# Kernel optimization log

Hardware: AMD Instinct MI355X
Metric: run time of the kernel (lower is better)

The kernel has to match this reference:

```python
import jax, jax.numpy as jnp
import numpy as np

B, N, C = 8, 4096, 512
K = 512   # key_channels
V = 512   # value_channels (must equal in_channels for reprojection to typecheck)
H = 8     # head_count


def setup_inputs() -> dict:
    key = jax.random.key(0)
    ks = jax.random.split(key, 10)
    s = 1.0 / np.sqrt(C)
    return {
        "input_": jax.random.normal(ks[0], (B, N, C), jnp.float32),
        "y": jax.random.normal(ks[1], (B, N, C), jnp.float32),
        "Wk": jax.random.uniform(ks[2], (C, K), jnp.float32, -s, s),
        "bk": jax.random.uniform(ks[3], (K,), jnp.float32, -s, s),
        "Wq": jax.random.uniform(ks[4], (C, K), jnp.float32, -s, s),
        "bq": jax.random.uniform(ks[5], (K,), jnp.float32, -s, s),
        "Wv": jax.random.uniform(ks[6], (C, K), jnp.float32, -s, s),
        "bv": jax.random.uniform(ks[7], (K,), jnp.float32, -s, s),
        "Wr": jax.random.uniform(ks[8], (C, K), jnp.float32, -s, s),
        "br": jax.random.uniform(ks[9], (K,), jnp.float32, -s, s),
    }


def reference(input_, y, Wk, bk, Wq, bq, Wv, bv, Wr, br):
    hk = K // H  # head key channels
    hv = V // H  # head value channels
    # projections -> [B, N, H, h]
    keys = ((input_ + y) @ Wk + bk).reshape(B, N, H, hk)
    queries = (y @ Wq + bq).reshape(B, N, H, hk)
    values = (input_ @ Wv + bv).reshape(B, N, H, hv)
    # key softmax over tokens N; query softmax over head channels hk
    keys = jax.nn.softmax(keys, axis=1)
    queries = jax.nn.softmax(queries, axis=3)
    # context[b,h,k,v] = sum_n key[b,n,h,k] * value[b,n,h,v]
    context = jnp.einsum('bnhk,bnhv->bhkv', keys, values)
    # attended[b,n,h,v] = sum_k context[b,h,k,v] * query[b,n,h,k]
    attended = jnp.einsum('bhkv,bnhk->bnhv', context, queries)
    aggregated = attended.reshape(B, N, V)  # concat heads over value channels
    return aggregated @ Wr + br
```

## Files before the change

### kernel.cpp

```cpp
#include <hip/hip_runtime.h>
#include <hip/hip_bf16.h>
#include <stdint.h>


typedef __attribute__((ext_vector_type(8))) short short8;
typedef __attribute__((ext_vector_type(4))) float f32x4;
typedef __attribute__((ext_vector_type(4))) unsigned short us4;

__device__ __forceinline__ unsigned short f2bf(float f) {
  union { float f; unsigned u; } v; v.f = f;
  unsigned r = v.u + 0x7FFFu + ((v.u >> 16) & 1u);
  return (unsigned short)(r >> 16);
}
__device__ __forceinline__ float bf2f(unsigned short u) {
  union { unsigned u; float f; } v; v.u = ((unsigned)u) << 16;
  return v.f;
}
__device__ __forceinline__ ushort2 pk2(float a, float b) {
  __hip_bfloat162 h = __float22bfloat162_rn(float2{a, b});
  return *reinterpret_cast<ushort2*>(&h);
}
__device__ __forceinline__ void gload16(const void* g, void* l) {
  __builtin_amdgcn_global_load_lds(
      (const __attribute__((address_space(1))) void*)g,
      (__attribute__((address_space(3))) void*)l, 16, 0, 0);
}

__global__ void prep_w(const float* __restrict__ Wk, const float* __restrict__ Wq,
                       const float* __restrict__ Wv, const float* __restrict__ Wr,
                       unsigned short* __restrict__ Wt) {
  __shared__ float tile[64][65];
  const int t = threadIdx.x;
  const int bx = blockIdx.x, by = blockIdx.y, w = blockIdx.z;
  const float* W = (w == 0) ? Wk : (w == 1) ? Wq : (w == 2) ? Wv : Wr;
  unsigned short* O = Wt + (size_t)w * 512 * 512;
#pragma unroll
  for (int p = 0; p < 16; ++p) {
    int idx = p * 256 + t; int r = idx >> 6, c = idx & 63;
    tile[r][c] = W[(size_t)(by * 64 + r) * 512 + bx * 64 + c];
  }
  __syncthreads();
#pragma unroll
  for (int p = 0; p < 16; ++p) {
    int idx = p * 256 + t; int r = idx >> 6, c = idx & 63;
    O[(size_t)(bx * 64 + r) * 512 + by * 64 + c] = f2bf(tile[c][r]);
  }
}

__global__ __launch_bounds__(256) void prep_xy(const float* __restrict__ x, const float* __restrict__ y,
                        unsigned short* __restrict__ xb, unsigned short* __restrict__ yb,
                        unsigned short* __restrict__ xyb) {
  const size_t i = ((size_t)blockIdx.x * 256 + threadIdx.x) * 16;
  float4 a[4], b[4];
#pragma unroll
  for (int q = 0; q < 4; ++q) a[q] = *(const float4*)(x + i + q * 4);
#pragma unroll
  for (int q = 0; q < 4; ++q) b[q] = *(const float4*)(y + i + q * 4);
#pragma unroll
  for (int h = 0; h < 2; ++h) {
    float4 a0 = a[2 * h], a1 = a[2 * h + 1], b0 = b[2 * h], b1 = b[2 * h + 1];
    short8 vx, vy, vs;
    ushort2 p;
    p = pk2(a0.x, a0.y); vx[0] = (short)p.x; vx[1] = (short)p.y;
    p = pk2(a0.z, a0.w); vx[2] = (short)p.x; vx[3] = (short)p.y;
    p = pk2(a1.x, a1.y); vx[4] = (short)p.x; vx[5] = (short)p.y;
    p = pk2(a1.z, a1.w); vx[6] = (short)p.x; vx[7] = (short)p.y;
    p = pk2(b0.x, b0.y); vy[0] = (short)p.x; vy[1] = (short)p.y;
    p = pk2(b0.z, b0.w); vy[2] = (short)p.x; vy[3] = (short)p.y;
    p = pk2(b1.x, b1.y); vy[4] = (short)p.x; vy[5] = (short)p.y;
    p = pk2(b1.z, b1.w); vy[6] = (short)p.x; vy[7] = (short)p.y;
    p = pk2(a0.x + b0.x, a0.y + b0.y); vs[0] = (short)p.x; vs[1] = (short)p.y;
    p = pk2(a0.z + b0.z, a0.w + b0.w); vs[2] = (short)p.x; vs[3] = (short)p.y;
    p = pk2(a1.x + b1.x, a1.y + b1.y); vs[4] = (short)p.x; vs[5] = (short)p.y;
    p = pk2(a1.z + b1.z, a1.w + b1.w); vs[6] = (short)p.x; vs[7] = (short)p.y;
    *(short8*)(xb + i + h * 8) = vx;
    *(short8*)(yb + i + h * 8) = vy;
    *(short8*)(xyb + i + h * 8) = vs;
  }
}

__global__ __launch_bounds__(256) void gemm_proj3(
    const unsigned short* __restrict__ xyb, const unsigned short* __restrict__ xb,
    const unsigned short* __restrict__ yb, const unsigned short* __restrict__ Wt,
    const float* __restrict__ bk, const float* __restrict__ bv, const float* __restrict__ bq,
    unsigned short* __restrict__ KeT, unsigned short* __restrict__ VT,
    unsigned short* __restrict__ Qp, float* __restrict__ S, int sec_off) {
  __shared__ __align__(16) unsigned short As[2][128][64];
  __shared__ __align__(16) unsigned short Bs[2][128][64];
  const int t = threadIdx.x, l = t & 63, w = t >> 6;
  const int lr = l & 15, lg = l >> 4;
  const int wr = w >> 1, wc = w & 1;
  const int sec = (int)(blockIdx.x >> 10) + sec_off;
  const int bid = blockIdx.x & 1023;
  const int swz = (bid & 7) * 128 + (bid >> 3);
  const int tn = swz & 3, tm = swz >> 2;

  const unsigned short* A = (sec == 0) ? xyb : (sec == 1) ? xb : yb;
  const unsigned short* Bbase = Wt + (size_t)((sec == 0) ? 0 : (sec == 1) ? 2 : 1) * 262144;
  const float* bias = (sec == 0) ? bk : (sec == 1) ? bv : bq;

  const int r0 = w * 8 + (l >> 3);
  const int su = ((l & 7) ^ (l >> 3)) * 8;
  const unsigned short* Ag = A + (size_t)(tm * 128 + r0) * 512 + su;
  const unsigned short* Bg = Bbase + (size_t)(tn * 128 + r0) * 512 + su;

  f32x4 acc[4][4] = {};

#define PSTAGE(buf, kt)                                                        \
  {                                                                            \
    _Pragma("unroll") for (int i = 0; i < 4; ++i) {                            \
      gload16(Ag + (size_t)i * 32 * 512 + (kt) * 64, &As[buf][i * 32 + w * 8][0]); \
      gload16(Bg + (size_t)i * 32 * 512 + (kt) * 64, &Bs[buf][i * 32 + w * 8][0]); \
    }                                                                          \
  }

  PSTAGE(0, 0)
  PSTAGE(1, 1)
  for (int kt = 0; kt < 8; ++kt) {
    const int cur = kt & 1;
    if (kt < 7) { asm volatile("s_waitcnt vmcnt(8)" ::: "memory"); }
    else        { asm volatile("s_waitcnt vmcnt(0)" ::: "memory"); }
    __builtin_amdgcn_s_barrier();
    asm volatile("" ::: "memory");
    __builtin_amdgcn_s_setprio(1);
#pragma unroll
    for (int kk = 0; kk < 2; ++kk) {
      short8 af[4], bf[4];
#pragma unroll
      for (int m = 0; m < 4; ++m)
        af[m] = *(const short8*)&As[cur][wr * 64 + m * 16 + lr][((kk * 4 + lg) ^ (lr & 7)) * 8];
#pragma unroll
      for (int n = 0; n < 4; ++n)
        bf[n] = *(const short8*)&Bs[cur][wc * 64 + n * 16 + lr][((kk * 4 + lg) ^ (lr & 7)) * 8];
#pragma unroll
      for (int m = 0; m < 4; ++m)
#pragma unroll
        for (int n = 0; n < 4; ++n)
          acc[m][n] = __builtin_amdgcn_mfma_f32_16x16x32_bf16(af[m], bf[n], acc[m][n], 0, 0, 0);
    }
    __builtin_amdgcn_s_setprio(0);
    asm volatile("" ::: "memory");
    __builtin_amdgcn_s_barrier();
    asm volatile("" ::: "memory");
    if (kt < 6) PSTAGE(cur, kt + 2)
  }
#undef PSTAGE

  const int c_base = tn * 128 + wc * 64;
  const int r_base = tm * 128 + wr * 64;
  float bv_[4];
#pragma unroll
  for (int n = 0; n < 4; ++n) bv_[n] = bias[c_base + n * 16 + lr];

  if (sec == 2) {
#pragma unroll
    for (int m = 0; m < 4; ++m) {
#pragma unroll
      for (int j = 0; j < 4; ++j) {
        float a0 = acc[m][0][j] + bv_[0], a1 = acc[m][1][j] + bv_[1];
        float a2 = acc[m][2][j] + bv_[2], a3 = acc[m][3][j] + bv_[3];
        float mx = fmaxf(fmaxf(a0, a1), fmaxf(a2, a3));
#pragma unroll
        for (int o = 1; o < 16; o <<= 1) mx = fmaxf(mx, __shfl_xor(mx, o));
        float e0 = __expf(a0 - mx), e1 = __expf(a1 - mx);
        float e2 = __expf(a2 - mx), e3 = __expf(a3 - mx);
        float s = e0 + e1 + e2 + e3;
#pragma unroll
        for (int o = 1; o < 16; o <<= 1) s += __shfl_xor(s, o);
        const float rs = 1.0f / s;
        const int row = r_base + m * 16 + lg * 4 + j;
        Qp[(size_t)row * 512 + c_base + 0 * 16 + lr] = f2bf(e0 * rs);
        Qp[(size_t)row * 512 + c_base + 1 * 16 + lr] = f2bf(e1 * rs);
        Qp[(size_t)row * 512 + c_base + 2 * 16 + lr] = f2bf(e2 * rs);
        Qp[(size_t)row * 512 + c_base + 3 * 16 + lr] = f2bf(e3 * rs);
      }
    }
  } else if (sec == 0) {
    const int b = (tm * 128) >> 12;
#pragma unroll
    for (int n = 0; n < 4; ++n) {
      const int col = c_base + n * 16 + lr;
      float srow = 0.f;
#pragma unroll
      for (int m = 0; m < 4; ++m) {
        const int row = r_base + m * 16 + lg * 4;
        const int nl = row & 4095;
        us4 v;
#pragma unroll
        for (int j = 0; j < 4; ++j) {
          float f = __expf(acc[m][n][j] + bv_[n]);
          srow += f;
          v[j] = f2bf(f);
        }
        *(us4*)&KeT[((size_t)(b * 512 + col)) * 4096 + nl] = v;
      }
      srow += __shfl_xor(srow, 16);
      srow += __shfl_xor(srow, 32);
      if (lg == 0) atomicAdd(&S[b * 512 + col], srow);
    }
  } else {
    const int b = (tm * 128) >> 12;
#pragma unroll
    for (int n = 0; n < 4; ++n) {
      const int col = c_base + n * 16 + lr;
#pragma unroll
      for (int m = 0; m < 4; ++m) {
        const int row = r_base + m * 16 + lg * 4;
        const int nl = row & 4095;
        us4 v;
#pragma unroll
        for (int j = 0; j < 4; ++j) v[j] = f2bf(acc[m][n][j] + bv_[n]);
        *(us4*)&VT[((size_t)(b * 512 + col)) * 4096 + nl] = v;
      }
    }
  }
}

__global__ void context_partial(const unsigned short* __restrict__ KeT,
                                const unsigned short* __restrict__ VT,
                                float* __restrict__ cp) {
  const int t = threadIdx.x, l = t & 63, w = t >> 6;
  const int lr = l & 15, lg = l >> 4;
  const int ch = blockIdx.x, h = blockIdx.y, b = blockIdx.z;
  const unsigned short* Kp = KeT + ((size_t)b * 512 + h * 64) * 4096;
  const unsigned short* Vp = VT + ((size_t)b * 512 + h * 64) * 4096;
  const int tok_w = ch * 1024 + w * 256;
  f32x4 acc[4][4] = {};
  for (int s = 0; s < 8; ++s) {
    const int tok = tok_w + s * 32 + lg * 8;
    short8 a[4], kf[4];
#pragma unroll
    for (int m = 0; m < 4; ++m) a[m] = *(const short8*)&Vp[(size_t)(m * 16 + lr) * 4096 + tok];
#pragma unroll
    for (int n = 0; n < 4; ++n) kf[n] = *(const short8*)&Kp[(size_t)(n * 16 + lr) * 4096 + tok];
#pragma unroll
    for (int m = 0; m < 4; ++m)
#pragma unroll
      for (int n = 0; n < 4; ++n)
        acc[m][n] = __builtin_amdgcn_mfma_f32_16x16x32_bf16(a[m], kf[n], acc[m][n], 0, 0, 0);
  }
  __shared__ float red[4][64][64];
#pragma unroll
  for (int m = 0; m < 4; ++m)
#pragma unroll
    for (int n = 0; n < 4; ++n)
#pragma unroll
      for (int j = 0; j < 4; ++j)
        red[w][m * 16 + lg * 4 + j][n * 16 + lr] = acc[m][n][j];
  __syncthreads();
  const int blk = (b * 8 + h) * 4 + ch;
  float* o = cp + (size_t)blk * 4096;
  for (int i = 0; i < 16; ++i) {
    int e = i * 256 + t;
    int v = e >> 6, k = e & 63;
    o[e] = red[0][v][k] + red[1][v][k] + red[2][v][k] + red[3][v][k];
  }
}

__global__ void ctx_reduce(const float* __restrict__ cp, const float* __restrict__ S,
                           unsigned short* __restrict__ ctxN) {
  const int bh = blockIdx.x, t = threadIdx.x;
  const float* p = cp + (size_t)bh * 4 * 4096;
  for (int i = 0; i < 16; ++i) {
    int e = i * 256 + t;
    float vsum = p[e] + p[4096 + e] + p[8192 + e] + p[12288 + e];
    int v = e >> 6, k = e & 63;
    ctxN[(size_t)bh * 4096 + k * 64 + v] = f2bf(vsum / S[bh * 64 + k]);
  }
}

__global__ void ctx_mm(const unsigned short* __restrict__ ctxN, const unsigned short* __restrict__ Wrt,
                       unsigned short* __restrict__ MT) {
  const int t = threadIdx.x, l = t & 63, w = t >> 6;
  const int lr = l & 15, lg = l >> 4;
  const int h = blockIdx.x, b = blockIdx.y;
  const unsigned short* Ap = ctxN + (size_t)(b * 8 + h) * 4096;
  f32x4 acc[4][8] = {};
  const int c0 = w * 128;
#pragma unroll
  for (int kk = 0; kk < 2; ++kk) {
    const int vb = kk * 32 + lg * 8;
    short8 a[4], bfr[8];
#pragma unroll
    for (int m = 0; m < 4; ++m) a[m] = *(const short8*)&Ap[(m * 16 + lr) * 64 + vb];
#pragma unroll
    for (int n = 0; n < 8; ++n) bfr[n] = *(const short8*)&Wrt[(size_t)(c0 + n * 16 + lr) * 512 + h * 64 + vb];
#pragma unroll
    for (int m = 0; m < 4; ++m)
#pragma unroll
      for (int n = 0; n < 8; ++n)
        acc[m][n] = __builtin_amdgcn_mfma_f32_16x16x32_bf16(a[m], bfr[n], acc[m][n], 0, 0, 0);
  }
#pragma unroll
  for (int n = 0; n < 8; ++n) {
    const int c = c0 + n * 16 + lr;
#pragma unroll
    for (int m = 0; m < 4; ++m) {
      const int k = m * 16 + lg * 4;
      us4 v;
#pragma unroll
      for (int j = 0; j < 4; ++j) v[j] = f2bf(acc[m][n][j]);
      *(us4*)&MT[((size_t)b * 512 + c) * 512 + h * 64 + k] = v;
    }
  }
}

__global__ __launch_bounds__(256) void gemm_final(const unsigned short* __restrict__ Qs,
                           const unsigned short* __restrict__ MT,
                           const float* __restrict__ br, float* __restrict__ out) {
  __shared__ __align__(16) unsigned short As[2][128][64];
  __shared__ __align__(16) unsigned short Bs[2][128][64];
  const int t = threadIdx.x, l = t & 63, w = t >> 6;
  const int lr = l & 15, lg = l >> 4;
  const int wr = w >> 1, wc = w & 1;
  const int bid = blockIdx.x;
  const int swz = (bid & 7) * 128 + (bid >> 3);
  const int tn = swz & 3, tm = swz >> 2;

  const unsigned short* Bbase = MT + (size_t)(tm >> 5) * 262144;
  const int r0 = w * 8 + (l >> 3);
  const int su = ((l & 7) ^ (l >> 3)) * 8;
  const unsigned short* Ag = Qs + (size_t)(tm * 128 + r0) * 512 + su;
  const unsigned short* Bg = Bbase + (size_t)(tn * 128 + r0) * 512 + su;

  f32x4 acc[4][4] = {};

#define PSTAGE(buf, kt)                                                        \
  {                                                                            \
    _Pragma("unroll") for (int i = 0; i < 4; ++i) {                            \
      gload16(Ag + (size_t)i * 32 * 512 + (kt) * 64, &As[buf][i * 32 + w * 8][0]); \
      gload16(Bg + (size_t)i * 32 * 512 + (kt) * 64, &Bs[buf][i * 32 + w * 8][0]); \
    }                                                                          \
  }

  PSTAGE(0, 0)
  PSTAGE(1, 1)
  for (int kt = 0; kt < 8; ++kt) {
    const int cur = kt & 1;
    if (kt < 7) { asm volatile("s_waitcnt vmcnt(8)" ::: "memory"); }
    else        { asm volatile("s_waitcnt vmcnt(0)" ::: "memory"); }
    __builtin_amdgcn_s_barrier();
    asm volatile("" ::: "memory");
    __builtin_amdgcn_s_setprio(1);
#pragma unroll
    for (int kk = 0; kk < 2; ++kk) {
      short8 af[4], bf[4];
#pragma unroll
      for (int m = 0; m < 4; ++m)
        af[m] = *(const short8*)&As[cur][wr * 64 + m * 16 + lr][((kk * 4 + lg) ^ (lr & 7)) * 8];
#pragma unroll
      for (int n = 0; n < 4; ++n)
        bf[n] = *(const short8*)&Bs[cur][wc * 64 + n * 16 + lr][((kk * 4 + lg) ^ (lr & 7)) * 8];
#pragma unroll
      for (int m = 0; m < 4; ++m)
#pragma unroll
        for (int n = 0; n < 4; ++n)
          acc[m][n] = __builtin_amdgcn_mfma_f32_16x16x32_bf16(af[m], bf[n], acc[m][n], 0, 0, 0);
    }
    __builtin_amdgcn_s_setprio(0);
    asm volatile("" ::: "memory");
    __builtin_amdgcn_s_barrier();
    asm volatile("" ::: "memory");
    if (kt < 6) PSTAGE(cur, kt + 2)
  }
#undef PSTAGE

  const int c_base = tn * 128 + wc * 64;
  const int r_base = tm * 128 + wr * 64;
#pragma unroll
  for (int n = 0; n < 4; ++n) {
    const int col = c_base + n * 16 + lr;
    const float bs = br[col];
#pragma unroll
    for (int m = 0; m < 4; ++m) {
      const int row = r_base + m * 16 + lg * 4;
#pragma unroll
      for (int j = 0; j < 4; ++j)
        out[(size_t)(row + j) * 512 + col] = acc[m][n][j] + bs;
    }
  }
}

extern "C" void kernel_launch(void* const* d_in, const int* in_sizes, int n_in,
                              void* d_out, int out_size, void* d_ws, size_t ws_size,
                              hipStream_t stream) {
  (void)in_sizes; (void)n_in; (void)out_size;
  const float* x  = (const float*)d_in[0];
  const float* y  = (const float*)d_in[1];
  const float* Wk = (const float*)d_in[2];
  const float* bk = (const float*)d_in[3];
  const float* Wq = (const float*)d_in[4];
  const float* bq = (const float*)d_in[5];
  const float* Wv = (const float*)d_in[6];
  const float* bv = (const float*)d_in[7];
  const float* Wr = (const float*)d_in[8];
  const float* br = (const float*)d_in[9];
  float* out = (float*)d_out;

  char* ws = (char*)d_ws;
  unsigned short* Wt   = (unsigned short*)(ws + 0);
  unsigned short* xb   = (unsigned short*)(ws + 2097152);
  unsigned short* yb   = (unsigned short*)(ws + 35651584);
  unsigned short* xyb  = (unsigned short*)(ws + 69206016);
  unsigned short* KeT  = (unsigned short*)(ws + 102760448);
  unsigned short* VT   = (unsigned short*)(ws + 136314880);
  float* S             = (float*)(ws + 169869312);
  float* cp            = (float*)(ws + 169885696);
  unsigned short* ctxN = (unsigned short*)(ws + 174080000);
  unsigned short* MT   = (unsigned short*)(ws + 174604288);
  unsigned short* QpX  = (unsigned short*)(ws + 178798592);
  const bool wide = ws_size >= (size_t)210364416;
  unsigned short* Qp   = wide ? QpX : xyb;

  prep_w<<<dim3(8, 8, 4), 256, 0, stream>>>(Wk, Wq, Wv, Wr, Wt);
  prep_xy<<<4096, 256, 0, stream>>>(x, y, xb, yb, xyb);
  hipMemsetAsync(S, 0, 512 * 8 * sizeof(float), stream);
  if (wide) {
    gemm_proj3<<<3072, 256, 0, stream>>>(xyb, xb, yb, Wt, bk, bv, bq, KeT, VT, Qp, S, 0);
  } else {
    gemm_proj3<<<2048, 256, 0, stream>>>(xyb, xb, yb, Wt, bk, bv, bq, KeT, VT, Qp, S, 0);
    gemm_proj3<<<1024, 256, 0, stream>>>(xyb, xb, yb, Wt, bk, bv, bq, KeT, VT, Qp, S, 2);
  }
  context_partial<<<dim3(4, 8, 8), 256, 0, stream>>>(KeT, VT, cp);
  ctx_reduce<<<64, 256, 0, stream>>>(cp, S, ctxN);
  ctx_mm<<<dim3(8, 8), 256, 0, stream>>>(ctxN, Wt + 3 * 262144, MT);
  gemm_final<<<1024, 256, 0, stream>>>(Qp, MT, br, out);
}
```

Baseline: 223.5 us.

## Fuse fp32-to-bf16 input conversion and x+y add into projection GEMM loads

```diff
diff --git a/kernel.cpp b/kernel.cpp
--- a/kernel.cpp
+++ b/kernel.cpp
@@ -47,61 +47,210 @@
   }
 }
 
-__global__ __launch_bounds__(256) void prep_xy(const float* __restrict__ x, const float* __restrict__ y,
-                        unsigned short* __restrict__ xb, unsigned short* __restrict__ yb,
-                        unsigned short* __restrict__ xyb) {
-  const size_t i = ((size_t)blockIdx.x * 256 + threadIdx.x) * 16;
-  float4 a[4], b[4];
-#pragma unroll
-  for (int q = 0; q < 4; ++q) a[q] = *(const float4*)(x + i + q * 4);
-#pragma unroll
-  for (int q = 0; q < 4; ++q) b[q] = *(const float4*)(y + i + q * 4);
-#pragma unroll
-  for (int h = 0; h < 2; ++h) {
-    float4 a0 = a[2 * h], a1 = a[2 * h + 1], b0 = b[2 * h], b1 = b[2 * h + 1];
-    short8 vx, vy, vs;
-    ushort2 p;
-    p = pk2(a0.x, a0.y); vx[0] = (short)p.x; vx[1] = (short)p.y;
-    p = pk2(a0.z, a0.w); vx[2] = (short)p.x; vx[3] = (short)p.y;
-    p = pk2(a1.x, a1.y); vx[4] = (short)p.x; vx[5] = (short)p.y;
-    p = pk2(a1.z, a1.w); vx[6] = (short)p.x; vx[7] = (short)p.y;
-    p = pk2(b0.x, b0.y); vy[0] = (short)p.x; vy[1] = (short)p.y;
-    p = pk2(b0.z, b0.w); vy[2] = (short)p.x; vy[3] = (short)p.y;
-    p = pk2(b1.x, b1.y); vy[4] = (short)p.x; vy[5] = (short)p.y;
-    p = pk2(b1.z, b1.w); vy[6] = (short)p.x; vy[7] = (short)p.y;
-    p = pk2(a0.x + b0.x, a0.y + b0.y); vs[0] = (short)p.x; vs[1] = (short)p.y;
-    p = pk2(a0.z + b0.z, a0.w + b0.w); vs[2] = (short)p.x; vs[3] = (short)p.y;
-    p = pk2(a1.x + b1.x, a1.y + b1.y); vs[4] = (short)p.x; vs[5] = (short)p.y;
-    p = pk2(a1.z + b1.z, a1.w + b1.w); vs[6] = (short)p.x; vs[7] = (short)p.y;
-    *(short8*)(xb + i + h * 8) = vx;
-    *(short8*)(yb + i + h * 8) = vy;
-    *(short8*)(xyb + i + h * 8) = vs;
-  }
-}
-
-__global__ __launch_bounds__(256) void gemm_proj3(
-    const unsigned short* __restrict__ xyb, const unsigned short* __restrict__ xb,
-    const unsigned short* __restrict__ yb, const unsigned short* __restrict__ Wt,
-    const float* __restrict__ bk, const float* __restrict__ bv, const float* __restrict__ bq,
-    unsigned short* __restrict__ KeT, unsigned short* __restrict__ VT,
-    unsigned short* __restrict__ Qp, float* __restrict__ S, int sec_off) {
+template <int MODE>
+__global__ __launch_bounds__(256) void gemm_projf(
+    const float* __restrict__ A0, const float* __restrict__ A1,
+    const unsigned short* __restrict__ Bt, const float* __restrict__ bias,
+    unsigned short* __restrict__ Out, float* __restrict__ S) {
   __shared__ __align__(16) unsigned short As[2][128][64];
   __shared__ __align__(16) unsigned short Bs[2][128][64];
   const int t = threadIdx.x, l = t & 63, w = t >> 6;
   const int lr = l & 15, lg = l >> 4;
   const int wr = w >> 1, wc = w & 1;
-  const int sec = (int)(blockIdx.x >> 10) + sec_off;
-  const int bid = blockIdx.x & 1023;
+  const int bid = blockIdx.x;
   const int swz = (bid & 7) * 128 + (bid >> 3);
   const int tn = swz & 3, tm = swz >> 2;
 
-  const unsigned short* A = (sec == 0) ? xyb : (sec == 1) ? xb : yb;
-  const unsigned short* Bbase = Wt + (size_t)((sec == 0) ? 0 : (sec == 1) ? 2 : 1) * 262144;
-  const float* bias = (sec == 0) ? bk : (sec == 1) ? bv : bq;
-
   const int r0 = w * 8 + (l >> 3);
   const int su = ((l & 7) ^ (l >> 3)) * 8;
-  const unsigned short* Ag = A + (size_t)(tm * 128 + r0) * 512 + su;
+  const unsigned short* Bg = Bt + (size_t)(tn * 128 + r0) * 512 + su;
+
+  const int ar = t >> 1, ah = t & 1;
+  const float* Ar0 = A0 + (size_t)(tm * 128 + ar) * 512 + ah * 32;
+  const float* Ar1 = (MODE == 0) ? (A1 + (size_t)(tm * 128 + ar) * 512 + ah * 32) : nullptr;
+
+  float4 ax[8], ay[8];
+  f32x4 acc[4][4] = {};
+
+#define FENCE asm volatile("" ::: "memory")
+#define ALOAD(kt)                                                              \
+  {                                                                            \
+    _Pragma("unroll") for (int i = 0; i < 8; ++i)                              \
+        ax[i] = *(const float4*)(Ar0 + (kt) * 64 + i * 4);                     \
+    if (MODE == 0) {                                                           \
+      _Pragma("unroll") for (int i = 0; i < 8; ++i)                            \
+          ay[i] = *(const float4*)(Ar1 + (kt) * 64 + i * 4);                   \
+    }                                                                          \
+  }
+#define AWRITE(buf)                                                            \
+  {                                                                            \
+    _Pragma("unroll") for (int iu = 0; iu < 4; ++iu) {                         \
+      float4 u0 = ax[2 * iu], u1 = ax[2 * iu + 1];                             \
+      if (MODE == 0) {                                                         \
+        float4 v0 = ay[2 * iu], v1 = ay[2 * iu + 1];                           \
+        u0.x += v0.x; u0.y += v0.y; u0.z += v0.z; u0.w += v0.w;                \
+        u1.x += v1.x; u1.y += v1.y; u1.z += v1.z; u1.w += v1.w;                \
+      }                                                                        \
+      ushort2 c0 = pk2(u0.x, u0.y), c1 = pk2(u0.z, u0.w);                      \
+      ushort2 c2 = pk2(u1.x, u1.y), c3 = pk2(u1.z, u1.w);                      \
+      short8 v;                                                                \
+      v[0] = (short)c0.x; v[1] = (short)c0.y; v[2] = (short)c1.x;              \
+      v[3] = (short)c1.y; v[4] = (short)c2.x; v[5] = (short)c2.y;              \
+      v[6] = (short)c3.x; v[7] = (short)c3.y;                                  \
+      *(short8*)&As[buf][ar][(((ah * 4 + iu) ^ (ar & 7)) * 8)] = v;            \
+    }                                                                          \
+  }
+#define BGISS(buf, kt)                                                         \
+  {                                                                            \
+    _Pragma("unroll") for (int i = 0; i < 4; ++i)                              \
+        gload16(Bg + (size_t)i * 32 * 512 + (kt) * 64, &Bs[buf][i * 32 + w * 8][0]); \
+  }
+#define WAIT_A asm volatile("s_waitcnt vmcnt(4)" ::: "memory")
+#define WAIT_B                                                                 \
+  {                                                                            \
+    if (MODE == 0) { asm volatile("s_waitcnt vmcnt(24)" ::: "memory"); }       \
+    else           { asm volatile("s_waitcnt vmcnt(16)" ::: "memory"); }       \
+  }
+
+  ALOAD(0); FENCE; BGISS(0, 0);
+  WAIT_A;
+  AWRITE(0);
+  FENCE; ALOAD(1); FENCE; BGISS(1, 1);
+  asm volatile("s_waitcnt lgkmcnt(0)" ::: "memory");
+  WAIT_B;
+  __builtin_amdgcn_s_barrier();
+  FENCE;
+
+  for (int kt = 0; kt < 8; ++kt) {
+    const int cur = kt & 1;
+    __builtin_amdgcn_s_setprio(1);
+#pragma unroll
+    for (int kk = 0; kk < 2; ++kk) {
+      short8 af[4], bf[4];
+#pragma unroll
+      for (int m = 0; m < 4; ++m)
+        af[m] = *(const short8*)&As[cur][wr * 64 + m * 16 + lr][((kk * 4 + lg) ^ (lr & 7)) * 8];
+#pragma unroll
+      for (int n = 0; n < 4; ++n)
+        bf[n] = *(const short8*)&Bs[cur][wc * 64 + n * 16 + lr][((kk * 4 + lg) ^ (lr & 7)) * 8];
+#pragma unroll
+      for (int m = 0; m < 4; ++m)
+#pragma unroll
+        for (int n = 0; n < 4; ++n)
+          acc[m][n] = __builtin_amdgcn_mfma_f32_16x16x32_bf16(af[m], bf[n], acc[m][n], 0, 0, 0);
+    }
+    __builtin_amdgcn_s_setprio(0);
+    FENCE;
+    if (kt < 7) {
+      WAIT_A;
+      AWRITE(cur ^ 1);
+      asm volatile("s_waitcnt lgkmcnt(0)" ::: "memory");
+      __builtin_amdgcn_s_barrier();
+      FENCE;
+      if (kt < 6) {
+        ALOAD(kt + 2); FENCE; BGISS(cur, kt + 2);
+        WAIT_B;
+      } else {
+        asm volatile("s_waitcnt vmcnt(0)" ::: "memory");
+      }
+      __builtin_amdgcn_s_barrier();
+      FENCE;
+    }
+  }
+  asm volatile("s_waitcnt vmcnt(0) lgkmcnt(0)" ::: "memory");
+#undef FENCE
+#undef ALOAD
+#undef AWRITE
+#undef BGISS
+#undef WAIT_A
+#undef WAIT_B
+
+  const int c_base = tn * 128 + wc * 64;
+  const int r_base = tm * 128 + wr * 64;
+  float bv_[4];
+#pragma unroll
+  for (int n = 0; n < 4; ++n) bv_[n] = bias[c_base + n * 16 + lr];
+
+  if (MODE == 1) {
+#pragma unroll
+    for (int m = 0; m < 4; ++m) {
+#pragma unroll
+      for (int j = 0; j < 4; ++j) {
+        float a0 = acc[m][0][j] + bv_[0], a1 = acc[m][1][j] + bv_[1];
+        float a2 = acc[m][2][j] + bv_[2], a3 = acc[m][3][j] + bv_[3];
+        float mx = fmaxf(fmaxf(a0, a1), fmaxf(a2, a3));
+#pragma unroll
+        for (int o = 1; o < 16; o <<= 1) mx = fmaxf(mx, __shfl_xor(mx, o));
+        float e0 = __expf(a0 - mx), e1 = __expf(a1 - mx);
+        float e2 = __expf(a2 - mx), e3 = __expf(a3 - mx);
+        float s = e0 + e1 + e2 + e3;
+#pragma unroll
+        for (int o = 1; o < 16; o <<= 1) s += __shfl_xor(s, o);
+        const float rs = 1.0f / s;
+        const int row = r_base + m * 16 + lg * 4 + j;
+        Out[(size_t)row * 512 + c_base + 0 * 16 + lr] = f2bf(e0 * rs);
+        Out[(size_t)row * 512 + c_base + 1 * 16 + lr] = f2bf(e1 * rs);
+        Out[(size_t)row * 512 + c_base + 2 * 16 + lr] = f2bf(e2 * rs);
+        Out[(size_t)row * 512 + c_base + 3 * 16 + lr] = f2bf(e3 * rs);
+      }
+    }
+  } else if (MODE == 0) {
+    const int b = (tm * 128) >> 12;
+#pragma unroll
+    for (int n = 0; n < 4; ++n) {
+      const int col = c_base + n * 16 + lr;
+      float srow = 0.f;
+#pragma unroll
+      for (int m = 0; m < 4; ++m) {
+        const int row = r_base + m * 16 + lg * 4;
+        const int nl = row & 4095;
+        us4 v;
+#pragma unroll
+        for (int j = 0; j < 4; ++j) {
+          float f = __expf(acc[m][n][j] + bv_[n]);
+          srow += f;
+          v[j] = f2bf(f);
+        }
+        *(us4*)&Out[((size_t)(b * 512 + col)) * 4096 + nl] = v;
+      }
+      srow += __shfl_xor(srow, 16);
+      srow += __shfl_xor(srow, 32);
+      if (lg == 0) atomicAdd(&S[b * 512 + col], srow);
+    }
+  } else {
+    const int b = (tm * 128) >> 12;
+#pragma unroll
+    for (int n = 0; n < 4; ++n) {
+      const int col = c_base + n * 16 + lr;
+#pragma unroll
+      for (int m = 0; m < 4; ++m) {
+        const int row = r_base + m * 16 + lg * 4;
+        const int nl = row & 4095;
+        us4 v;
+#pragma unroll
+        for (int j = 0; j < 4; ++j) v[j] = f2bf(acc[m][n][j] + bv_[n]);
+        *(us4*)&Out[((size_t)(b * 512 + col)) * 4096 + nl] = v;
+      }
+    }
+  }
+}
+
+__global__ __launch_bounds__(256) void gemm_final(const unsigned short* __restrict__ Qs,
+                           const unsigned short* __restrict__ MT,
+                           const float* __restrict__ br, float* __restrict__ out) {
+  __shared__ __align__(16) unsigned short As[2][128][64];
+  __shared__ __align__(16) unsigned short Bs[2][128][64];
+  const int t = threadIdx.x, l = t & 63, w = t >> 6;
+  const int lr = l & 15, lg = l >> 4;
+  const int wr = w >> 1, wc = w & 1;
+  const int bid = blockIdx.x;
+  const int swz = (bid & 7) * 128 + (bid >> 3);
+  const int tn = swz & 3, tm = swz >> 2;
+
+  const unsigned short* Bbase = MT + (size_t)(tm >> 5) * 262144;
+  const int r0 = w * 8 + (l >> 3);
+  const int su = ((l & 7) ^ (l >> 3)) * 8;
+  const unsigned short* Ag = Qs + (size_t)(tm * 128 + r0) * 512 + su;
   const unsigned short* Bg = Bbase + (size_t)(tn * 128 + r0) * 512 + su;
 
   f32x4 acc[4][4] = {};
@@ -148,70 +297,16 @@
 
   const int c_base = tn * 128 + wc * 64;
   const int r_base = tm * 128 + wr * 64;
-  float bv_[4];
-#pragma unroll
-  for (int n = 0; n < 4; ++n) bv_[n] = bias[c_base + n * 16 + lr];
-
-  if (sec == 2) {
+#pragma unroll
+  for (int n = 0; n < 4; ++n) {
+    const int col = c_base + n * 16 + lr;
+    const float bs = br[col];
 #pragma unroll
     for (int m = 0; m < 4; ++m) {
-#pragma unroll
-      for (int j = 0; j < 4; ++j) {
-        float a0 = acc[m][0][j] + bv_[0], a1 = acc[m][1][j] + bv_[1];
-        float a2 = acc[m][2][j] + bv_[2], a3 = acc[m][3][j] + bv_[3];
-        float mx = fmaxf(fmaxf(a0, a1), fmaxf(a2, a3));
-#pragma unroll
-        for (int o = 1; o < 16; o <<= 1) mx = fmaxf(mx, __shfl_xor(mx, o));
-        float e0 = __expf(a0 - mx), e1 = __expf(a1 - mx);
-        float e2 = __expf(a2 - mx), e3 = __expf(a3 - mx);
-        float s = e0 + e1 + e2 + e3;
-#pragma unroll
-        for (int o = 1; o < 16; o <<= 1) s += __shfl_xor(s, o);
-        const float rs = 1.0f / s;
-        const int row = r_base + m * 16 + lg * 4 + j;
-        Qp[(size_t)row * 512 + c_base + 0 * 16 + lr] = f2bf(e0 * rs);
-        Qp[(size_t)row * 512 + c_base + 1 * 16 + lr] = f2bf(e1 * rs);
-        Qp[(size_t)row * 512 + c_base + 2 * 16 + lr] = f2bf(e2 * rs);
-        Qp[(size_t)row * 512 + c_base + 3 * 16 + lr] = f2bf(e3 * rs);
-      }
-    }
-  } else if (sec == 0) {
-    const int b = (tm * 128) >> 12;
-#pragma unroll
-    for (int n = 0; n < 4; ++n) {
-      const int col = c_base + n * 16 + lr;
-      float srow = 0.f;
-#pragma unroll
-      for (int m = 0; m < 4; ++m) {
-        const int row = r_base + m * 16 + lg * 4;
-        const int nl = row & 4095;
-        us4 v;
-#pragma unroll
-        for (int j = 0; j < 4; ++j) {
-          float f = __expf(acc[m][n][j] + bv_[n]);
-          srow += f;
-          v[j] = f2bf(f);
-        }
-        *(us4*)&KeT[((size_t)(b * 512 + col)) * 4096 + nl] = v;
-      }
-      srow += __shfl_xor(srow, 16);
-      srow += __shfl_xor(srow, 32);
-      if (lg == 0) atomicAdd(&S[b * 512 + col], srow);
-    }
-  } else {
-    const int b = (tm * 128) >> 12;
-#pragma unroll
-    for (int n = 0; n < 4; ++n) {
-      const int col = c_base + n * 16 + lr;
-#pragma unroll
-      for (int m = 0; m < 4; ++m) {
-        const int row = r_base + m * 16 + lg * 4;
-        const int nl = row & 4095;
-        us4 v;
-#pragma unroll
-        for (int j = 0; j < 4; ++j) v[j] = f2bf(acc[m][n][j] + bv_[n]);
-        *(us4*)&VT[((size_t)(b * 512 + col)) * 4096 + nl] = v;
-      }
+      const int row = r_base + m * 16 + lg * 4;
+#pragma unroll
+      for (int j = 0; j < 4; ++j)
+        out[(size_t)(row + j) * 512 + col] = acc[m][n][j] + bs;
     }
   }
 }
@@ -305,86 +400,10 @@
   }
 }
 
-__global__ __launch_bounds__(256) void gemm_final(const unsigned short* __restrict__ Qs,
-                           const unsigned short* __restrict__ MT,
-                           const float* __restrict__ br, float* __restrict__ out) {
-  __shared__ __align__(16) unsigned short As[2][128][64];
-  __shared__ __align__(16) unsigned short Bs[2][128][64];
-  const int t = threadIdx.x, l = t & 63, w = t >> 6;
-  const int lr = l & 15, lg = l >> 4;
-  const int wr = w >> 1, wc = w & 1;
-  const int bid = blockIdx.x;
-  const int swz = (bid & 7) * 128 + (bid >> 3);
-  const int tn = swz & 3, tm = swz >> 2;
-
-  const unsigned short* Bbase = MT + (size_t)(tm >> 5) * 262144;
-  const int r0 = w * 8 + (l >> 3);
-  const int su = ((l & 7) ^ (l >> 3)) * 8;
-  const unsigned short* Ag = Qs + (size_t)(tm * 128 + r0) * 512 + su;
-  const unsigned short* Bg = Bbase + (size_t)(tn * 128 + r0) * 512 + su;
-
-  f32x4 acc[4][4] = {};
-
-#define PSTAGE(buf, kt)                                                        \
-  {                                                                            \
-    _Pragma("unroll") for (int i = 0; i < 4; ++i) {                            \
-      gload16(Ag + (size_t)i * 32 * 512 + (kt) * 64, &As[buf][i * 32 + w * 8][0]); \
-      gload16(Bg + (size_t)i * 32 * 512 + (kt) * 64, &Bs[buf][i * 32 + w * 8][0]); \
-    }                                                                          \
-  }
-
-  PSTAGE(0, 0)
-  PSTAGE(1, 1)
-  for (int kt = 0; kt < 8; ++kt) {
-    const int cur = kt & 1;
-    if (kt < 7) { asm volatile("s_waitcnt vmcnt(8)" ::: "memory"); }
-    else        { asm volatile("s_waitcnt vmcnt(0)" ::: "memory"); }
-    __builtin_amdgcn_s_barrier();
-    asm volatile("" ::: "memory");
-    __builtin_amdgcn_s_setprio(1);
-#pragma unroll
-    for (int kk = 0; kk < 2; ++kk) {
-      short8 af[4], bf[4];
-#pragma unroll
-      for (int m = 0; m < 4; ++m)
-        af[m] = *(const short8*)&As[cur][wr * 64 + m * 16 + lr][((kk * 4 + lg) ^ (lr & 7)) * 8];
-#pragma unroll
-      for (int n = 0; n < 4; ++n)
-        bf[n] = *(const short8*)&Bs[cur][wc * 64 + n * 16 + lr][((kk * 4 + lg) ^ (lr & 7)) * 8];
-#pragma unroll
-      for (int m = 0; m < 4; ++m)
-#pragma unroll
-        for (int n = 0; n < 4; ++n)
-          acc[m][n] = __builtin_amdgcn_mfma_f32_16x16x32_bf16(af[m], bf[n], acc[m][n], 0, 0, 0);
-    }
-    __builtin_amdgcn_s_setprio(0);
-    asm volatile("" ::: "memory");
-    __builtin_amdgcn_s_barrier();
-    asm volatile("" ::: "memory");
-    if (kt < 6) PSTAGE(cur, kt + 2)
-  }
-#undef PSTAGE
-
-  const int c_base = tn * 128 + wc * 64;
-  const int r_base = tm * 128 + wr * 64;
-#pragma unroll
-  for (int n = 0; n < 4; ++n) {
-    const int col = c_base + n * 16 + lr;
-    const float bs = br[col];
-#pragma unroll
-    for (int m = 0; m < 4; ++m) {
-      const int row = r_base + m * 16 + lg * 4;
-#pragma unroll
-      for (int j = 0; j < 4; ++j)
-        out[(size_t)(row + j) * 512 + col] = acc[m][n][j] + bs;
-    }
-  }
-}
-
 extern "C" void kernel_launch(void* const* d_in, const int* in_sizes, int n_in,
                               void* d_out, int out_size, void* d_ws, size_t ws_size,
                               hipStream_t stream) {
-  (void)in_sizes; (void)n_in; (void)out_size;
+  (void)in_sizes; (void)n_in; (void)out_size; (void)ws_size;
   const float* x  = (const float*)d_in[0];
   const float* y  = (const float*)d_in[1];
   const float* Wk = (const float*)d_in[2];
@@ -399,28 +418,19 @@
 
   char* ws = (char*)d_ws;
   unsigned short* Wt   = (unsigned short*)(ws + 0);
-  unsigned short* xb   = (unsigned short*)(ws + 2097152);
-  unsigned short* yb   = (unsigned short*)(ws + 35651584);
-  unsigned short* xyb  = (unsigned short*)(ws + 69206016);
-  unsigned short* KeT  = (unsigned short*)(ws + 102760448);
-  unsigned short* VT   = (unsigned short*)(ws + 136314880);
-  float* S             = (float*)(ws + 169869312);
-  float* cp            = (float*)(ws + 169885696);
-  unsigned short* ctxN = (unsigned short*)(ws + 174080000);
-  unsigned short* MT   = (unsigned short*)(ws + 174604288);
-  unsigned short* QpX  = (unsigned short*)(ws + 178798592);
-  const bool wide = ws_size >= (size_t)210364416;
-  unsigned short* Qp   = wide ? QpX : xyb;
+  unsigned short* KeT  = (unsigned short*)(ws + 2097152);
+  unsigned short* VT   = (unsigned short*)(ws + 35651584);
+  unsigned short* Qp   = (unsigned short*)(ws + 69206016);
+  float* S             = (float*)(ws + 102760448);
+  float* cp            = (float*)(ws + 102776832);
+  unsigned short* ctxN = (unsigned short*)(ws + 106971136);
+  unsigned short* MT   = (unsigned short*)(ws + 107495424);
 
   prep_w<<<dim3(8, 8, 4), 256, 0, stream>>>(Wk, Wq, Wv, Wr, Wt);
-  prep_xy<<<4096, 256, 0, stream>>>(x, y, xb, yb, xyb);
   hipMemsetAsync(S, 0, 512 * 8 * sizeof(float), stream);
-  if (wide) {
-    gemm_proj3<<<3072, 256, 0, stream>>>(xyb, xb, yb, Wt, bk, bv, bq, KeT, VT, Qp, S, 0);
-  } else {
-    gemm_proj3<<<2048, 256, 0, stream>>>(xyb, xb, yb, Wt, bk, bv, bq, KeT, VT, Qp, S, 0);
-    gemm_proj3<<<1024, 256, 0, stream>>>(xyb, xb, yb, Wt, bk, bv, bq, KeT, VT, Qp, S, 2);
-  }
+  gemm_projf<0><<<1024, 256, 0, stream>>>(x, y, Wt, bk, KeT, S);
+  gemm_projf<2><<<1024, 256, 0, stream>>>(x, nullptr, Wt + 2 * 262144, bv, VT, nullptr);
+  gemm_projf<1><<<1024, 256, 0, stream>>>(y, nullptr, Wt + 262144, bq, Qp, nullptr);
   context_partial<<<dim3(4, 8, 8), 256, 0, stream>>>(KeT, VT, cp);
   ctx_reduce<<<64, 256, 0, stream>>>(cp, S, ctxN);
   ctx_mm<<<dim3(8, 8), 256, 0, stream>>>(ctxN, Wt + 3 * 262144, MT);
```

Result: slower. 288.6 us (+29.2%).
